# Kernel optimization log

Hardware: AMD Instinct MI355X
Metric: run time of the kernel (lower is better)

Reference implementation:

```python
import jax, jax.numpy as jnp
import numpy as np

D_MODEL = 512
NUM_HEADS = 8
D_K = D_MODEL // NUM_HEADS
D_FF = 4 * D_MODEL
EPS = 1e-5


def _pos_encoding(seq_len, d_model, dtype=jnp.float32):
    pos = jnp.arange(seq_len, dtype=jnp.float32)[:, None]              # [S,1]
    div = jnp.exp(jnp.arange(0, d_model, 2, dtype=jnp.float32) * (-np.log(10000.0) / d_model))  # [D/2]
    ang = pos * div                                                      # [S,D/2]
    pe = jnp.stack([jnp.sin(ang), jnp.cos(ang)], axis=-1).reshape(seq_len, d_model)
    return pe.astype(dtype)


def _layernorm(x, g, b):
    mu = jnp.mean(x, axis=-1, keepdims=True)
    var = jnp.mean(jnp.square(x - mu), axis=-1, keepdims=True)
    return (x - mu) * jax.lax.rsqrt(var + EPS) * g + b


def setup_inputs() -> dict:
    key = jax.random.key(0)
    ks = jax.random.split(key, 12)
    B, S, D = 4, 2048, D_MODEL
    s = 1.0 / np.sqrt(D)
    inp = {
        "x": jax.random.normal(ks[0], (B, S, D), jnp.float32),
        "Wq": jax.random.normal(ks[1], (D, D), jnp.float32) * s,
        "bq": jnp.zeros((D,), jnp.float32),
        "Wk": jax.random.normal(ks[2], (D, D), jnp.float32) * s,
        "bk": jnp.zeros((D,), jnp.float32),
        "Wv": jax.random.normal(ks[3], (D, D), jnp.float32) * s,
        "bv": jnp.zeros((D,), jnp.float32),
        "Wo": jax.random.normal(ks[4], (D, D), jnp.float32) * s,
        "bo": jnp.zeros((D,), jnp.float32),
        "g1": jnp.ones((D,), jnp.float32),
        "b1": jnp.zeros((D,), jnp.float32),
        "W_ff1": jax.random.normal(ks[5], (D, D_FF), jnp.float32) * s,
        "b_ff1": jnp.zeros((D_FF,), jnp.float32),
        "W_ff2": jax.random.normal(ks[6], (D_FF, D), jnp.float32) * (1.0 / np.sqrt(D_FF)),
        "b_ff2": jnp.zeros((D,), jnp.float32),
        "g2": jnp.ones((D,), jnp.float32),
        "b2": jnp.zeros((D,), jnp.float32),
    }
    return inp


def reference(x, Wq, bq, Wk, bk, Wv, bv, Wo, bo, g1, b1, W_ff1, b_ff1, W_ff2, b_ff2, g2, b2):
    B, S, D = x.shape
    H, dk = NUM_HEADS, D_K
    # positional encoding (deterministic buffer)
    x = x + _pos_encoding(S, D, x.dtype)[None]
    # projections -> [B,H,S,dk]
    q = (x @ Wq + bq).reshape(B, S, H, dk).transpose(0, 2, 1, 3)
    k = (x @ Wk + bk).reshape(B, S, H, dk).transpose(0, 2, 1, 3)
    v = (x @ Wv + bv).reshape(B, S, H, dk).transpose(0, 2, 1, 3)
    # naive attention: materialized [B,H,S,S] scores (as in original)
    scores = jnp.einsum('bhqd,bhkd->bhqk', q, k) / np.sqrt(dk)
    attn = jax.nn.softmax(scores, axis=-1)
    ctx = jnp.einsum('bhqk,bhkd->bhqd', attn, v)
    ctx = ctx.transpose(0, 2, 1, 3).reshape(B, S, D)
    attn_out = ctx @ Wo + bo
    # residual + LN + FFN + residual + LN
    h = _layernorm(x + attn_out, g1, b1)
    ff = jax.nn.relu(h @ W_ff1 + b_ff1) @ W_ff2 + b_ff2
    return _layernorm(h + ff, g2, b2)
```

## Files before the change

kernel.cpp:

```cpp
#include <hip/hip_runtime.h>

typedef unsigned short u16;
typedef unsigned int u32;
typedef __attribute__((ext_vector_type(8))) short s16x8;
typedef __attribute__((ext_vector_type(2))) float f32x2;
typedef __attribute__((ext_vector_type(4))) float f32x4;
typedef __attribute__((ext_vector_type(16))) float f32x16;
typedef __attribute__((ext_vector_type(2))) u32 u32x2;
typedef __attribute__((ext_vector_type(4))) u32 u32x4;

#define MB (1ull << 20)
#define K1SCALE 0.18033688f

__device__ __forceinline__ u16 f2bf(float f) {
  u32 u = __float_as_uint(f);
  u32 r = (u + 0x7fffu + ((u >> 16) & 1u)) >> 16;
  return (u16)r;
}

__device__ __forceinline__ float bf2f(u16 x) { return __uint_as_float(((u32)x) << 16); }

__device__ __forceinline__ u32 cvtpk(float lo, float hi) {
  u32 r;
  asm("v_cvt_pk_bf16_f32 %0, %1, %2" : "=v"(r) : "v"(lo), "v"(hi));
  return r;
}

__device__ __forceinline__ float max3f(float a, float b, float c) {
  float d;
  asm("v_max3_f32 %0, %1, %2, %3" : "=v"(d) : "v"(a), "v"(b), "v"(c));
  return d;
}

__device__ __forceinline__ f32x2 pk_mul(f32x2 a, f32x2 b) {
  f32x2 d;
  asm("v_pk_mul_f32 %0, %1, %2" : "=v"(d) : "v"(a), "v"(b));
  return d;
}
__device__ __forceinline__ f32x2 pk_add(f32x2 a, f32x2 b) {
  f32x2 d;
  asm("v_pk_add_f32 %0, %1, %2" : "=v"(d) : "v"(a), "v"(b));
  return d;
}

__device__ __forceinline__ void gload16(const u16* g, u16* l) {
  __builtin_amdgcn_global_load_lds((const __attribute__((address_space(1))) void*)g,
                                   (__attribute__((address_space(3))) void*)l, 16, 0, 0);
}

__global__ __launch_bounds__(256) void k_posenc(const float* __restrict__ x,
                                                float* __restrict__ xf, u16* __restrict__ xb) {
  int idx = blockIdx.x * 256 + threadIdx.x;
  int col = idx & 511;
  int srow = (idx >> 9) & 2047;
  int i2 = col >> 1;
  float div = expf((float)i2 * -0.03597789207803196f);
  float ang = (float)srow * div;
  float pe = (col & 1) ? cosf(ang) : sinf(ang);
  float v = x[idx] + pe;
  xf[idx] = v;
  xb[idx] = f2bf(v);
}

__global__ __launch_bounds__(256) void k_tcast(const float* __restrict__ W, u16* __restrict__ Wt,
                                               int K, int N, float scale) {
  __shared__ float tile[32][33];
  int k0 = blockIdx.x * 32, n0 = blockIdx.y * 32;
  int tx = threadIdx.x & 31, ty = threadIdx.x >> 5;
  #pragma unroll
  for (int i = 0; i < 32; i += 8)
    tile[ty + i][tx] = W[(size_t)(k0 + ty + i) * N + n0 + tx];
  __syncthreads();
  #pragma unroll
  for (int i = 0; i < 32; i += 8)
    Wt[(size_t)(n0 + ty + i) * K + k0 + tx] = f2bf(tile[tx][ty + i] * scale);
}

__global__ void k_cat3(const float* __restrict__ a, const float* __restrict__ b,
                       const float* __restrict__ c, float* __restrict__ o, float sa) {
  int t = blockIdx.x * 256 + threadIdx.x;
  float v = (t < 512) ? a[t] * sa : ((t < 1024) ? b[t - 512] : c[t - 1024]);
  o[t] = v;
}

#define GBM 128
#define GBK 64

template <bool RELU, bool WF32, bool WBF16>
__global__ __launch_bounds__(256) void k_gemm(const u16* __restrict__ A, const u16* __restrict__ Bt,
                                              const float* __restrict__ bias,
                                              float* __restrict__ Cf, u16* __restrict__ Cb,
                                              int N, int K) {
  __shared__ u16 lA[GBM * GBK];
  __shared__ u16 lB[GBM * GBK];
  int t = threadIdx.x;
  int lane = t & 63;
  int w = t >> 6;
  int wm = w >> 1, wn = w & 1;
  int g = lane >> 4, c = lane & 15;
  size_t tm = (size_t)blockIdx.x * GBM;
  size_t tn = (size_t)blockIdx.y * GBM;

  f32x4 acc[4][4];
  #pragma unroll
  for (int i = 0; i < 4; i++)
    #pragma unroll
    for (int j = 0; j < 4; j++) acc[i][j] = (f32x4){0.f, 0.f, 0.f, 0.f};

  for (int k0 = 0; k0 < K; k0 += GBK) {
    __syncthreads();
    #pragma unroll
    for (int i = 0; i < 4; i++) {
      int ch = t + i * 256;
      int row = ch >> 3;
      int koff = ((ch ^ row) & 7) << 3;
      gload16(A + (tm + row) * K + k0 + koff, lA + ch * 8);
      gload16(Bt + (tn + row) * K + k0 + koff, lB + ch * 8);
    }
    __syncthreads();
    #pragma unroll
    for (int kh = 0; kh < 2; kh++) {
      int sl = ((g + 4 * kh) ^ (c & 7)) << 3;
      s16x8 af[4], bf[4];
      #pragma unroll
      for (int i = 0; i < 4; i++) {
        af[i] = *(const s16x8*)&lA[(wm * 64 + i * 16 + c) * GBK + sl];
        bf[i] = *(const s16x8*)&lB[(wn * 64 + i * 16 + c) * GBK + sl];
      }
      #pragma unroll
      for (int i = 0; i < 4; i++)
        #pragma unroll
        for (int j = 0; j < 4; j++)
          acc[i][j] = __builtin_amdgcn_mfma_f32_16x16x32_bf16(af[i], bf[j], acc[i][j], 0, 0, 0);
    }
  }
  #pragma unroll
  for (int j = 0; j < 4; j++) {
    size_t col = tn + wn * 64 + j * 16 + c;
    float bv = bias[col];
    #pragma unroll
    for (int i = 0; i < 4; i++) {
      size_t row0 = tm + wm * 64 + i * 16 + g * 4;
      #pragma unroll
      for (int r = 0; r < 4; r++) {
        float v = acc[i][j][r] + bv;
        if (RELU) v = fmaxf(v, 0.0f);
        if (WF32) Cf[(row0 + r) * N + col] = v;
        if (WBF16) Cb[(row0 + r) * N + col] = f2bf(v);
      }
    }
  }
}

__global__ __launch_bounds__(256) void k_vt(const u16* __restrict__ qkv, u16* __restrict__ vT) {
  __shared__ u16 tile[32][33];
  int bh = blockIdx.z;
  int b = bh >> 3, h = bh & 7;
  int s0 = blockIdx.x * 32, d0 = blockIdx.y * 32;
  int tx = threadIdx.x & 31, ty = threadIdx.x >> 5;
  #pragma unroll
  for (int i = 0; i < 32; i += 8)
    tile[ty + i][tx] = qkv[(size_t)(b * 2048 + s0 + ty + i) * 1536 + 1024 + h * 64 + d0 + tx];
  __syncthreads();
  #pragma unroll
  for (int i = 0; i < 32; i += 8)
    vT[(size_t)(bh * 64 + d0 + ty + i) * 2048 + s0 + tx] = tile[tx][ty + i];
}

union F16U {
  f32x16 v;
  f32x2 p[8];
};

__global__ __launch_bounds__(512, 4) void k_attn(const u16* __restrict__ qkv,
                                                 const u16* __restrict__ vT,
                                                 u16* __restrict__ ctx) {
  __shared__ u16 lds[8][4096];
  int t = threadIdx.x;
  int w = t >> 6, lane = t & 63;
  int qg = w >> 1, kh = w & 1;
  int ql = lane & 31, hi = lane >> 5;
  int bh = blockIdx.y;
  int b = bh >> 3, h = bh & 7;
  int q0 = blockIdx.x * 128 + qg * 32;
  int r7 = ql & 7;

  int sh = t >> 8;
  int th = t & 255;
  const u16* kbaseg = qkv + (size_t)(b * 2048 + sh * 1024) * 1536 + 512 + h * 64;
  const u16* vbaseg = vT + (size_t)(bh * 64) * 2048 + sh * 1024;

  auto stage = [&](int buf, int step) {
    int t0 = step * 64;
    #pragma unroll
    for (int i = 0; i < 2; i++) {
      int ch = th + i * 256;
      int row = ch >> 3;
      int off = ((ch ^ row) & 7) << 3;
      gload16(kbaseg + (size_t)(t0 + row) * 1536 + off, &lds[(sh * 2 + buf) * 2][ch * 8]);
      gload16(vbaseg + (size_t)row * 2048 + t0 + off, &lds[(sh * 2 + buf) * 2 + 1][ch * 8]);
    }
  };

  const u16* qbase = qkv + (size_t)(b * 2048 + q0 + ql) * 1536 + h * 64 + hi * 8;
  s16x8 qf[4];
  #pragma unroll
  for (int ks = 0; ks < 4; ks++) qf[ks] = *(const s16x8*)(qbase + ks * 16);

  float m = -1e30f, l = 0.f;
  F16U O0, O1;
  #pragma unroll
  for (int i = 0; i < 16; i++) { O0.v[i] = 0.f; O1.v[i] = 0.f; }

  stage(0, 0);

  for (int step = 0; step < 16; ++step) {
    int buf = step & 1;
    asm volatile("s_waitcnt vmcnt(0)" ::: "memory");
    __builtin_amdgcn_s_barrier();
    __builtin_amdgcn_sched_barrier(0);
    if (step < 15) stage(buf ^ 1, step + 1);

    const u16* lK = lds[(kh * 2 + buf) * 2];
    const u16* lV = lds[(kh * 2 + buf) * 2 + 1];

    F16U S0, S1;
    #pragma unroll
    for (int i = 0; i < 16; i++) { S0.v[i] = 0.f; S1.v[i] = 0.f; }
    #pragma unroll
    for (int ks = 0; ks < 4; ks++) {
      int so = ((ks * 2 + hi) ^ r7) << 3;
      s16x8 kf0 = *(const s16x8*)&lK[ql * 64 + so];
      s16x8 kf1 = *(const s16x8*)&lK[(32 + ql) * 64 + so];
      S0.v = __builtin_amdgcn_mfma_f32_32x32x16_bf16(kf0, qf[ks], S0.v, 0, 0, 0);
      S1.v = __builtin_amdgcn_mfma_f32_32x32x16_bf16(kf1, qf[ks], S1.v, 0, 0, 0);
    }

    float a0 = max3f(S0.v[0], S0.v[1], S0.v[2]);
    float a1 = max3f(S0.v[3], S0.v[4], S0.v[5]);
    float a2 = max3f(S0.v[6], S0.v[7], S0.v[8]);
    float a3 = max3f(S0.v[9], S0.v[10], S0.v[11]);
    float a4 = max3f(S0.v[12], S0.v[13], S0.v[14]);
    float a5 = max3f(S0.v[15], S1.v[0], S1.v[1]);
    float a6 = max3f(S1.v[2], S1.v[3], S1.v[4]);
    float a7 = max3f(S1.v[5], S1.v[6], S1.v[7]);
    float a8 = max3f(S1.v[8], S1.v[9], S1.v[10]);
    float a9 = max3f(S1.v[11], S1.v[12], S1.v[13]);
    float a10 = fmaxf(S1.v[14], S1.v[15]);
    float b0 = max3f(a0, a1, a2);
    float b1 = max3f(a3, a4, a5);
    float b2 = max3f(a6, a7, a8);
    float b3 = max3f(a9, a10, b0);
    float rm = max3f(b1, b2, b3);
    rm = fmaxf(rm, __shfl_xor(rm, 32, 64));

    if (!__all(rm <= m + 8.0f)) {
      float mn = fmaxf(m, rm);
      float al = __builtin_amdgcn_exp2f(m - mn);
      m = mn;
      f32x2 alp = {al, al};
      #pragma unroll
      for (int i = 0; i < 8; i++) {
        O0.p[i] = pk_mul(O0.p[i], alp);
        O1.p[i] = pk_mul(O1.p[i], alp);
      }
      l *= al;
    }

    f32x2 nmp = {-m, -m};
    #pragma unroll
    for (int i = 0; i < 8; i++) {
      S0.p[i] = pk_add(S0.p[i], nmp);
      S1.p[i] = pk_add(S1.p[i], nmp);
    }
    #pragma unroll
    for (int i = 0; i < 16; i++) {
      S0.v[i] = __builtin_amdgcn_exp2f(S0.v[i]);
      S1.v[i] = __builtin_amdgcn_exp2f(S1.v[i]);
    }
    f32x2 c0 = pk_add(S0.p[0], S0.p[1]);
    f32x2 c1 = pk_add(S0.p[2], S0.p[3]);
    f32x2 c2 = pk_add(S0.p[4], S0.p[5]);
    f32x2 c3 = pk_add(S0.p[6], S0.p[7]);
    f32x2 d0 = pk_add(S1.p[0], S1.p[1]);
    f32x2 d1 = pk_add(S1.p[2], S1.p[3]);
    f32x2 d2 = pk_add(S1.p[4], S1.p[5]);
    f32x2 d3 = pk_add(S1.p[6], S1.p[7]);
    c0 = pk_add(c0, c1);
    c2 = pk_add(c2, c3);
    d0 = pk_add(d0, d1);
    d2 = pk_add(d2, d3);
    c0 = pk_add(c0, c2);
    d0 = pk_add(d0, d2);
    c0 = pk_add(c0, d0);
    float pssum = c0[0] + c0[1];
    pssum += __shfl_xor(pssum, 32, 64);
    l += pssum;

    auto pv = [&](const f32x16& sv, int kb) {
      u32 a0w = cvtpk(sv[0], sv[1]), a1w = cvtpk(sv[2], sv[3]);
      u32 a2w = cvtpk(sv[4], sv[5]), a3w = cvtpk(sv[6], sv[7]);
      u32 b0w = cvtpk(sv[8], sv[9]), b1w = cvtpk(sv[10], sv[11]);
      u32 b2w = cvtpk(sv[12], sv[13]), b3w = cvtpk(sv[14], sv[15]);
      asm("v_permlane32_swap_b32 %0, %1" : "+v"(a0w), "+v"(a2w));
      asm("v_permlane32_swap_b32 %0, %1" : "+v"(a1w), "+v"(a3w));
      asm("v_permlane32_swap_b32 %0, %1" : "+v"(b0w), "+v"(b2w));
      asm("v_permlane32_swap_b32 %0, %1" : "+v"(b1w), "+v"(b3w));
      u32x4 w0v = {a0w, a1w, a2w, a3w};
      u32x4 w1v = {b0w, b1w, b2w, b3w};
      s16x8 pf0 = __builtin_bit_cast(s16x8, w0v);
      s16x8 pf1 = __builtin_bit_cast(s16x8, w1v);
      int base0 = ((kb * 4 + hi) ^ r7) << 3;
      int base1 = ((kb * 4 + 2 + hi) ^ r7) << 3;
      s16x8 vf00 = *(const s16x8*)&lV[ql * 64 + base0];
      s16x8 vf01 = *(const s16x8*)&lV[ql * 64 + base1];
      s16x8 vf10 = *(const s16x8*)&lV[(32 + ql) * 64 + base0];
      s16x8 vf11 = *(const s16x8*)&lV[(32 + ql) * 64 + base1];
      O0.v = __builtin_amdgcn_mfma_f32_32x32x16_bf16(vf00, pf0, O0.v, 0, 0, 0);
      O0.v = __builtin_amdgcn_mfma_f32_32x32x16_bf16(vf01, pf1, O0.v, 0, 0, 0);
      O1.v = __builtin_amdgcn_mfma_f32_32x32x16_bf16(vf10, pf0, O1.v, 0, 0, 0);
      O1.v = __builtin_amdgcn_mfma_f32_32x32x16_bf16(vf11, pf1, O1.v, 0, 0, 0);
    };
    pv(S0.v, 0);
    pv(S1.v, 1);
  }

  asm volatile("s_waitcnt lgkmcnt(0)" ::: "memory");
  __builtin_amdgcn_s_barrier();
  float* mrg = (float*)&lds[0][0];
  float* p = mrg + (size_t)(qg * 64 + lane) * 36;
  if (kh == 1) {
    p[0] = m;
    p[1] = l;
    #pragma unroll
    for (int i = 0; i < 16; i++) {
      p[2 + i] = O0.v[i];
      p[18 + i] = O1.v[i];
    }
  }
  asm volatile("s_waitcnt lgkmcnt(0)" ::: "memory");
  __builtin_amdgcn_s_barrier();
  if (kh == 0) {
    float m1 = p[0], l1 = p[1];
    float M = fmaxf(m, m1);
    float sc0 = __builtin_amdgcn_exp2f(m - M);
    float sc1 = __builtin_amdgcn_exp2f(m1 - M);
    float L = sc0 * l + sc1 * l1;
    float inv = 1.0f / L;
    sc0 *= inv;
    sc1 *= inv;
    size_t obase = (size_t)(b * 2048 + q0 + ql) * 512 + h * 64;
    #pragma unroll
    for (int k = 0; k < 4; k++) {
      float v0 = O0.v[4 * k] * sc0 + p[2 + 4 * k] * sc1;
      float v1 = O0.v[4 * k + 1] * sc0 + p[2 + 4 * k + 1] * sc1;
      float v2 = O0.v[4 * k + 2] * sc0 + p[2 + 4 * k + 2] * sc1;
      float v3 = O0.v[4 * k + 3] * sc0 + p[2 + 4 * k + 3] * sc1;
      u32x2 p0 = {cvtpk(v0, v1), cvtpk(v2, v3)};
      *(u32x2*)&ctx[obase + 8 * k + 4 * hi] = p0;
      float u0 = O1.v[4 * k] * sc0 + p[18 + 4 * k] * sc1;
      float u1 = O1.v[4 * k + 1] * sc0 + p[18 + 4 * k + 1] * sc1;
      float u2 = O1.v[4 * k + 2] * sc0 + p[18 + 4 * k + 2] * sc1;
      float u3 = O1.v[4 * k + 3] * sc0 + p[18 + 4 * k + 3] * sc1;
      u32x2 p1 = {cvtpk(u0, u1), cvtpk(u2, u3)};
      *(u32x2*)&ctx[obase + 32 + 8 * k + 4 * hi] = p1;
    }
  }
}

template <bool WB>
__global__ __launch_bounds__(256) void k_addln(const float* __restrict__ A, const float* __restrict__ Bv,
                                               const float* __restrict__ G, const float* __restrict__ Bb,
                                               float* __restrict__ Of, u16* __restrict__ Ob) {
  int row = blockIdx.x;
  int t = threadIdx.x;
  size_t base = (size_t)row * 512;
  float x0 = A[base + t] + Bv[base + t];
  float x1 = A[base + t + 256] + Bv[base + t + 256];
  float s = x0 + x1;
  #pragma unroll
  for (int d = 1; d < 64; d <<= 1) s += __shfl_xor(s, d, 64);
  __shared__ float red[8];
  int w = t >> 6, lane = t & 63;
  if (lane == 0) red[w] = s;
  __syncthreads();
  float mu = (red[0] + red[1] + red[2] + red[3]) * (1.0f / 512.0f);
  float d0 = x0 - mu, d1 = x1 - mu;
  float vs = d0 * d0 + d1 * d1;
  #pragma unroll
  for (int d = 1; d < 64; d <<= 1) vs += __shfl_xor(vs, d, 64);
  if (lane == 0) red[4 + w] = vs;
  __syncthreads();
  float var = (red[4] + red[5] + red[6] + red[7]) * (1.0f / 512.0f);
  float rs = rsqrtf(var + 1e-5f);
  float o0 = d0 * rs * G[t] + Bb[t];
  float o1 = d1 * rs * G[t + 256] + Bb[t + 256];
  Of[base + t] = o0;
  Of[base + t + 256] = o1;
  if (WB) {
    Ob[base + t] = f2bf(o0);
    Ob[base + t + 256] = f2bf(o1);
  }
}

extern "C" void kernel_launch(void* const* d_in, const int* in_sizes, int n_in,
                              void* d_out, int out_size, void* d_ws, size_t ws_size,
                              hipStream_t stream) {
  const float* x = (const float*)d_in[0];
  const float* Wq = (const float*)d_in[1];
  const float* bq = (const float*)d_in[2];
  const float* Wk = (const float*)d_in[3];
  const float* bk = (const float*)d_in[4];
  const float* Wv = (const float*)d_in[5];
  const float* bv = (const float*)d_in[6];
  const float* Wo = (const float*)d_in[7];
  const float* bo = (const float*)d_in[8];
  const float* g1 = (const float*)d_in[9];
  const float* b1 = (const float*)d_in[10];
  const float* Wff1 = (const float*)d_in[11];
  const float* bff1 = (const float*)d_in[12];
  const float* Wff2 = (const float*)d_in[13];
  const float* bff2 = (const float*)d_in[14];
  const float* g2 = (const float*)d_in[15];
  const float* b2 = (const float*)d_in[16];

  char* ws = (char*)d_ws;
  float* xpe_f = (float*)(ws + 0);
  u16* xpe_b = (u16*)(ws + 16 * MB);
  u16* qkv = (u16*)(ws + 24 * MB);
  u16* vT = (u16*)(ws + 48 * MB);
  u16* ctx = (u16*)(ws + 56 * MB);
  float* ao = (float*)(ws + 64 * MB);
  float* hf = (float*)(ws + 80 * MB);
  u16* hb = (u16*)(ws + 96 * MB);
  u16* ff1 = (u16*)(ws + 24 * MB);
  u16* WqkvT = (u16*)(ws + 104 * MB);
  u16* WoT = (u16*)(ws + 106 * MB);
  u16* Wff1T = (u16*)(ws + 107 * MB);
  u16* Wff2T = (u16*)(ws + 109 * MB);
  float* bqkv = (float*)(ws + 111 * MB);
  (void)in_sizes; (void)n_in; (void)out_size; (void)ws_size;

  k_posenc<<<16384, 256, 0, stream>>>(x, xpe_f, xpe_b);
  k_tcast<<<dim3(16, 16), 256, 0, stream>>>(Wq, WqkvT, 512, 512, K1SCALE);
  k_tcast<<<dim3(16, 16), 256, 0, stream>>>(Wk, WqkvT + 512 * 512, 512, 512, 1.0f);
  k_tcast<<<dim3(16, 16), 256, 0, stream>>>(Wv, WqkvT + 2 * 512 * 512, 512, 512, 1.0f);
  k_tcast<<<dim3(16, 16), 256, 0, stream>>>(Wo, WoT, 512, 512, 1.0f);
  k_tcast<<<dim3(16, 64), 256, 0, stream>>>(Wff1, Wff1T, 512, 2048, 1.0f);
  k_tcast<<<dim3(64, 16), 256, 0, stream>>>(Wff2, Wff2T, 2048, 512, 1.0f);
  k_cat3<<<6, 256, 0, stream>>>(bq, bk, bv, bqkv, K1SCALE);

  k_gemm<false, false, true><<<dim3(64, 12), 256, 0, stream>>>(xpe_b, WqkvT, bqkv, nullptr, qkv, 1536, 512);
  k_vt<<<dim3(64, 2, 32), 256, 0, stream>>>(qkv, vT);
  k_attn<<<dim3(16, 32), 512, 0, stream>>>(qkv, vT, ctx);
  k_gemm<false, true, false><<<dim3(64, 4), 256, 0, stream>>>(ctx, WoT, bo, ao, nullptr, 512, 512);
  k_addln<true><<<8192, 256, 0, stream>>>(xpe_f, ao, g1, b1, hf, hb);
  k_gemm<true, false, true><<<dim3(64, 16), 256, 0, stream>>>(hb, Wff1T, bff1, nullptr, ff1, 2048, 512);
  k_gemm<false, true, false><<<dim3(64, 4), 256, 0, stream>>>(ff1, Wff2T, bff2, ao, nullptr, 512, 2048);
  k_addln<false><<<8192, 256, 0, stream>>>(hf, ao, g2, b2, (float*)d_out, nullptr);
}
```

Before: 213.1 us.

## Merge weight-prep launches, vectorize elementwise kernels, use narrower GEMM tiles for N=512

Seven weight transpose/cast and bias-concat launches become one k_wprep kernel. The posenc and add-layernorm kernels now process two adjacent elements per thread with vector loads, packed bf16 conversion and fast sin/cos/exp intrinsics. The GEMM is templated on the N tile width, and the two N=512 GEMMs use 64-wide tiles so they launch 512 blocks instead of 256. This cuts launch overhead and improves occupancy for the narrow GEMMs, at the cost of some accuracy from the fast transcendentals.

```diff
diff --git a/kernel.cpp b/kernel.cpp
--- a/kernel.cpp
+++ b/kernel.cpp
@@ -51,21 +51,59 @@
 __global__ __launch_bounds__(256) void k_posenc(const float* __restrict__ x,
                                                 float* __restrict__ xf, u16* __restrict__ xb) {
   int idx = blockIdx.x * 256 + threadIdx.x;
-  int col = idx & 511;
-  int srow = (idx >> 9) & 2047;
-  int i2 = col >> 1;
-  float div = expf((float)i2 * -0.03597789207803196f);
+  int i2 = idx & 255;
+  int srow = (idx >> 8) & 2047;
+  float div = __expf((float)i2 * -0.03597789207803196f);
   float ang = (float)srow * div;
-  float pe = (col & 1) ? cosf(ang) : sinf(ang);
-  float v = x[idx] + pe;
-  xf[idx] = v;
-  xb[idx] = f2bf(v);
-}
-
-__global__ __launch_bounds__(256) void k_tcast(const float* __restrict__ W, u16* __restrict__ Wt,
-                                               int K, int N, float scale) {
+  f32x2 xv = *(const f32x2*)&x[(size_t)idx * 2];
+  float v0 = xv[0] + __sinf(ang);
+  float v1 = xv[1] + __cosf(ang);
+  *(f32x2*)&xf[(size_t)idx * 2] = (f32x2){v0, v1};
+  *(u32*)&xb[(size_t)idx * 2] = cvtpk(v0, v1);
+}
+
+__global__ __launch_bounds__(256) void k_wprep(const float* __restrict__ Wq, const float* __restrict__ Wk,
+                                               const float* __restrict__ Wv, const float* __restrict__ Wo,
+                                               const float* __restrict__ Wff1, const float* __restrict__ Wff2,
+                                               const float* __restrict__ bq, const float* __restrict__ bk,
+                                               const float* __restrict__ bv,
+                                               u16* __restrict__ WqkvT, u16* __restrict__ WoT,
+                                               u16* __restrict__ Wff1T, u16* __restrict__ Wff2T,
+                                               float* __restrict__ bqkv) {
   __shared__ float tile[32][33];
-  int k0 = blockIdx.x * 32, n0 = blockIdx.y * 32;
+  int id = blockIdx.x;
+  if (id >= 3072) {
+    int j = (id - 3072) * 256 + threadIdx.x;
+    float v = (j < 512) ? bq[j] * K1SCALE : ((j < 1024) ? bk[j - 512] : bv[j - 1024]);
+    bqkv[j] = v;
+    return;
+  }
+  const float* W;
+  u16* Wt;
+  int K, N, k0, n0;
+  float sc = 1.0f;
+  if (id < 1024) {
+    int mi = id >> 8, t = id & 255;
+    K = 512; N = 512;
+    k0 = (t & 15) * 32;
+    n0 = (t >> 4) * 32;
+    if (mi == 0) { W = Wq; Wt = WqkvT; sc = K1SCALE; }
+    else if (mi == 1) { W = Wk; Wt = WqkvT + 512 * 512; }
+    else if (mi == 2) { W = Wv; Wt = WqkvT + 2 * 512 * 512; }
+    else { W = Wo; Wt = WoT; }
+  } else if (id < 2048) {
+    int t = id - 1024;
+    K = 512; N = 2048;
+    k0 = (t & 15) * 32;
+    n0 = (t >> 4) * 32;
+    W = Wff1; Wt = Wff1T;
+  } else {
+    int t = id - 2048;
+    K = 2048; N = 512;
+    k0 = (t >> 4) * 32;
+    n0 = (t & 15) * 32;
+    W = Wff2; Wt = Wff2T;
+  }
   int tx = threadIdx.x & 31, ty = threadIdx.x >> 5;
   #pragma unroll
   for (int i = 0; i < 32; i += 8)
@@ -73,41 +111,32 @@
   __syncthreads();
   #pragma unroll
   for (int i = 0; i < 32; i += 8)
-    Wt[(size_t)(n0 + ty + i) * K + k0 + tx] = f2bf(tile[tx][ty + i] * scale);
-}
-
-__global__ void k_cat3(const float* __restrict__ a, const float* __restrict__ b,
-                       const float* __restrict__ c, float* __restrict__ o, float sa) {
-  int t = blockIdx.x * 256 + threadIdx.x;
-  float v = (t < 512) ? a[t] * sa : ((t < 1024) ? b[t - 512] : c[t - 1024]);
-  o[t] = v;
-}
-
-#define GBM 128
-#define GBK 64
-
-template <bool RELU, bool WF32, bool WBF16>
+    Wt[(size_t)(n0 + ty + i) * K + k0 + tx] = f2bf(tile[tx][ty + i] * sc);
+}
+
+template <int BN, bool RELU, bool WF32, bool WBF16>
 __global__ __launch_bounds__(256) void k_gemm(const u16* __restrict__ A, const u16* __restrict__ Bt,
                                               const float* __restrict__ bias,
                                               float* __restrict__ Cf, u16* __restrict__ Cb,
                                               int N, int K) {
-  __shared__ u16 lA[GBM * GBK];
-  __shared__ u16 lB[GBM * GBK];
+  constexpr int NACC = BN / 32;
+  __shared__ u16 lA[128 * 64];
+  __shared__ u16 lB[BN * 64];
   int t = threadIdx.x;
   int lane = t & 63;
   int w = t >> 6;
   int wm = w >> 1, wn = w & 1;
   int g = lane >> 4, c = lane & 15;
-  size_t tm = (size_t)blockIdx.x * GBM;
-  size_t tn = (size_t)blockIdx.y * GBM;
-
-  f32x4 acc[4][4];
+  size_t tm = (size_t)blockIdx.x * 128;
+  size_t tn = (size_t)blockIdx.y * BN;
+
+  f32x4 acc[4][NACC];
   #pragma unroll
   for (int i = 0; i < 4; i++)
     #pragma unroll
-    for (int j = 0; j < 4; j++) acc[i][j] = (f32x4){0.f, 0.f, 0.f, 0.f};
-
-  for (int k0 = 0; k0 < K; k0 += GBK) {
+    for (int j = 0; j < NACC; j++) acc[i][j] = (f32x4){0.f, 0.f, 0.f, 0.f};
+
+  for (int k0 = 0; k0 < K; k0 += 64) {
     __syncthreads();
     #pragma unroll
     for (int i = 0; i < 4; i++) {
@@ -115,28 +144,35 @@
       int row = ch >> 3;
       int koff = ((ch ^ row) & 7) << 3;
       gload16(A + (tm + row) * K + k0 + koff, lA + ch * 8);
+    }
+    #pragma unroll
+    for (int i = 0; i < BN / 32; i++) {
+      int ch = t + i * 256;
+      int row = ch >> 3;
+      int koff = ((ch ^ row) & 7) << 3;
       gload16(Bt + (tn + row) * K + k0 + koff, lB + ch * 8);
     }
     __syncthreads();
     #pragma unroll
     for (int kh = 0; kh < 2; kh++) {
       int sl = ((g + 4 * kh) ^ (c & 7)) << 3;
-      s16x8 af[4], bf[4];
+      s16x8 af[4], bf[NACC];
       #pragma unroll
-      for (int i = 0; i < 4; i++) {
-        af[i] = *(const s16x8*)&lA[(wm * 64 + i * 16 + c) * GBK + sl];
-        bf[i] = *(const s16x8*)&lB[(wn * 64 + i * 16 + c) * GBK + sl];
-      }
+      for (int i = 0; i < 4; i++)
+        af[i] = *(const s16x8*)&lA[(wm * 64 + i * 16 + c) * 64 + sl];
+      #pragma unroll
+      for (int j = 0; j < NACC; j++)
+        bf[j] = *(const s16x8*)&lB[(wn * (BN / 2) + j * 16 + c) * 64 + sl];
       #pragma unroll
       for (int i = 0; i < 4; i++)
         #pragma unroll
-        for (int j = 0; j < 4; j++)
+        for (int j = 0; j < NACC; j++)
           acc[i][j] = __builtin_amdgcn_mfma_f32_16x16x32_bf16(af[i], bf[j], acc[i][j], 0, 0, 0);
     }
   }
   #pragma unroll
-  for (int j = 0; j < 4; j++) {
-    size_t col = tn + wn * 64 + j * 16 + c;
+  for (int j = 0; j < NACC; j++) {
+    size_t col = tn + wn * (BN / 2) + j * 16 + c;
     float bv = bias[col];
     #pragma unroll
     for (int i = 0; i < 4; i++) {
@@ -374,9 +410,11 @@
                                                float* __restrict__ Of, u16* __restrict__ Ob) {
   int row = blockIdx.x;
   int t = threadIdx.x;
-  size_t base = (size_t)row * 512;
-  float x0 = A[base + t] + Bv[base + t];
-  float x1 = A[base + t + 256] + Bv[base + t + 256];
+  size_t base = (size_t)row * 512 + 2 * t;
+  f32x2 av = *(const f32x2*)&A[base];
+  f32x2 bv = *(const f32x2*)&Bv[base];
+  float x0 = av[0] + bv[0];
+  float x1 = av[1] + bv[1];
   float s = x0 + x1;
   #pragma unroll
   for (int d = 1; d < 64; d <<= 1) s += __shfl_xor(s, d, 64);
@@ -393,14 +431,12 @@
   __syncthreads();
   float var = (red[4] + red[5] + red[6] + red[7]) * (1.0f / 512.0f);
   float rs = rsqrtf(var + 1e-5f);
-  float o0 = d0 * rs * G[t] + Bb[t];
-  float o1 = d1 * rs * G[t + 256] + Bb[t + 256];
-  Of[base + t] = o0;
-  Of[base + t + 256] = o1;
-  if (WB) {
-    Ob[base + t] = f2bf(o0);
-    Ob[base + t + 256] = f2bf(o1);
-  }
+  f32x2 gg = *(const f32x2*)&G[2 * t];
+  f32x2 bb = *(const f32x2*)&Bb[2 * t];
+  float o0 = d0 * rs * gg[0] + bb[0];
+  float o1 = d1 * rs * gg[1] + bb[1];
+  *(f32x2*)&Of[base] = (f32x2){o0, o1};
+  if (WB) *(u32*)&Ob[base] = cvtpk(o0, o1);
 }
 
 extern "C" void kernel_launch(void* const* d_in, const int* in_sizes, int n_in,
@@ -441,21 +477,16 @@
   float* bqkv = (float*)(ws + 111 * MB);
   (void)in_sizes; (void)n_in; (void)out_size; (void)ws_size;
 
-  k_posenc<<<16384, 256, 0, stream>>>(x, xpe_f, xpe_b);
-  k_tcast<<<dim3(16, 16), 256, 0, stream>>>(Wq, WqkvT, 512, 512, K1SCALE);
-  k_tcast<<<dim3(16, 16), 256, 0, stream>>>(Wk, WqkvT + 512 * 512, 512, 512, 1.0f);
-  k_tcast<<<dim3(16, 16), 256, 0, stream>>>(Wv, WqkvT + 2 * 512 * 512, 512, 512, 1.0f);
-  k_tcast<<<dim3(16, 16), 256, 0, stream>>>(Wo, WoT, 512, 512, 1.0f);
-  k_tcast<<<dim3(16, 64), 256, 0, stream>>>(Wff1, Wff1T, 512, 2048, 1.0f);
-  k_tcast<<<dim3(64, 16), 256, 0, stream>>>(Wff2, Wff2T, 2048, 512, 1.0f);
-  k_cat3<<<6, 256, 0, stream>>>(bq, bk, bv, bqkv, K1SCALE);
-
-  k_gemm<false, false, true><<<dim3(64, 12), 256, 0, stream>>>(xpe_b, WqkvT, bqkv, nullptr, qkv, 1536, 512);
+  k_posenc<<<8192, 256, 0, stream>>>(x, xpe_f, xpe_b);
+  k_wprep<<<3078, 256, 0, stream>>>(Wq, Wk, Wv, Wo, Wff1, Wff2, bq, bk, bv,
+                                    WqkvT, WoT, Wff1T, Wff2T, bqkv);
+
+  k_gemm<128, false, false, true><<<dim3(64, 12), 256, 0, stream>>>(xpe_b, WqkvT, bqkv, nullptr, qkv, 1536, 512);
   k_vt<<<dim3(64, 2, 32), 256, 0, stream>>>(qkv, vT);
   k_attn<<<dim3(16, 32), 512, 0, stream>>>(qkv, vT, ctx);
-  k_gemm<false, true, false><<<dim3(64, 4), 256, 0, stream>>>(ctx, WoT, bo, ao, nullptr, 512, 512);
+  k_gemm<64, false, true, false><<<dim3(64, 8), 256, 0, stream>>>(ctx, WoT, bo, ao, nullptr, 512, 512);
   k_addln<true><<<8192, 256, 0, stream>>>(xpe_f, ao, g1, b1, hf, hb);
-  k_gemm<true, false, true><<<dim3(64, 16), 256, 0, stream>>>(hb, Wff1T, bff1, nullptr, ff1, 2048, 512);
-  k_gemm<false, true, false><<<dim3(64, 4), 256, 0, stream>>>(ff1, Wff2T, bff2, ao, nullptr, 512, 2048);
+  k_gemm<128, true, false, true><<<dim3(64, 16), 256, 0, stream>>>(hb, Wff1T, bff1, nullptr, ff1, 2048, 512);
+  k_gemm<64, false, true, false><<<dim3(64, 8), 256, 0, stream>>>(ff1, Wff2T, bff2, ao, nullptr, 512, 2048);
   k_addln<false><<<8192, 256, 0, stream>>>(hf, ao, g2, b2, (float*)d_out, nullptr);
 }
```

Measured after the change: 189.9 us. -10.9%, faster.
